# Kernel optimization log

Hardware: AMD Instinct MI355X
Metric: run time of the kernel (lower is better)

The kernel has to match this reference:

```python
import jax, jax.numpy as jnp
import numpy as np

B, N, C = 8, 1024, 1024
H = 16
D = C // H  # head_dim = 64


def apply_rope(t, cos, sin):
    # t: (B,H,N,D), cos/sin: (N, D//2). Interleaved-pair RoPE
    # (matches repeat_interleave(2) + stack(-y2,y1) in the torch code).
    tr = t.reshape(*t.shape[:-1], D // 2, 2)
    t1, t2 = tr[..., 0], tr[..., 1]
    o1 = t1 * cos - t2 * sin
    o2 = t2 * cos + t1 * sin
    return jnp.stack((o1, o2), axis=-1).reshape(t.shape)


def setup_inputs() -> dict:
    key = jax.random.key(0)
    k1, k2, k3, k4 = jax.random.split(key, 4)
    s = 0.02
    x = jax.random.normal(k1, (B, N, C), dtype=jnp.float32)
    w_qkv = jax.random.normal(k2, (C, 3 * C), dtype=jnp.float32) * s  # qkv_bias=False
    w_proj = jax.random.normal(k3, (C, C), dtype=jnp.float32) * s
    b_proj = jax.random.normal(k4, (C,), dtype=jnp.float32) * s
    return {"x": x, "w_qkv": w_qkv, "w_proj": w_proj, "b_proj": b_proj}


def reference(x, w_qkv, w_proj, b_proj):
    # QKV projection: (B,N,3C) -> (3,B,H,N,D)
    qkv = (x @ w_qkv).reshape(B, N, 3, H, D).transpose(2, 0, 3, 1, 4)
    q, k, v = qkv[0], qkv[1], qkv[2]

    # RoPE tables: pos = arange(N) (mask=None, no cls/registers)
    pos = jnp.arange(N, dtype=jnp.float32)
    omega = 1.0 / (10000.0 ** (jnp.arange(D // 2, dtype=jnp.float32) / (D / 2.0)))
    freq = pos[:, None] * omega  # (N, D//2)
    cos, sin = jnp.cos(freq), jnp.sin(freq)

    q = apply_rope(q, cos, sin)
    k = apply_rope(k, cos, sin)

    # Scaled dot-product attention (non-causal, no dropout in eval)
    scale = 1.0 / jnp.sqrt(jnp.float32(D))
    scores = jnp.einsum('bhqd,bhkd->bhqk', q, k) * scale
    attn = jax.nn.softmax(scores, axis=-1)
    out = jnp.einsum('bhqk,bhkd->bhqd', attn, v)

    # Merge heads + output projection
    out = out.transpose(0, 2, 1, 3).reshape(B, N, C)
    return out @ w_proj + b_proj
```

## Files before the change

### kernel.cpp

```cpp
#include <hip/hip_runtime.h>
#include <hip/hip_bf16.h>
#include <math.h>

#define Bsz  8
#define Nseq 1024
#define Cdim 1024
#define Hh   16
#define Dd   64

typedef short short8 __attribute__((ext_vector_type(8)));
typedef float floatx4 __attribute__((ext_vector_type(4)));

__device__ __forceinline__ unsigned short f2bf(float f) {
    __hip_bfloat16 h = __float2bfloat16(f);
    return __builtin_bit_cast(unsigned short, h);
}
__device__ __forceinline__ float b2f(unsigned short u) {
    return __uint_as_float(((unsigned)u) << 16);
}

__device__ __forceinline__ void async16(const void* g, void* l) {
    __builtin_amdgcn_global_load_lds(
        (const __attribute__((address_space(1))) unsigned int*)g,
        (__attribute__((address_space(3))) unsigned int*)l, 16, 0, 0);
}

__device__ __forceinline__ unsigned pack_bf16(float lo, float hi) {
    unsigned ulo = __float_as_uint(lo) + 0x8000u;
    unsigned uhi = __float_as_uint(hi) + 0x8000u;
    return __builtin_amdgcn_perm(uhi, ulo, 0x07060302);
}

__global__ __launch_bounds__(256) void rope_table(float2* __restrict__ tbl)
{
    int i = blockIdx.x * 256 + threadIdx.x;
    int n = i >> 5, p = i & 31;
    float omega = __expf(-(float)p * 0.2878231366242557f);
    float sv, cv;
    sincosf((float)n * omega, &sv, &cv);
    tbl[i] = make_float2(cv, sv);
}

__global__ __launch_bounds__(256) void convert_bf16(
    const float* __restrict__ in, unsigned short* __restrict__ out)
{
    int i = blockIdx.x * 256 + threadIdx.x;
    float4 v = ((const float4*)in)[i];
    ushort4 u;
    u.x = f2bf(v.x); u.y = f2bf(v.y); u.z = f2bf(v.z); u.w = f2bf(v.w);
    ((ushort4*)out)[i] = u;
}

__global__ __launch_bounds__(256) void transpose_bf16(
    const float* __restrict__ in, unsigned short* __restrict__ out, int R, int Ccols)
{
    __shared__ float T[64][65];
    int c0 = blockIdx.x * 64, r0 = blockIdx.y * 64;
    for (int i = threadIdx.x; i < 4096; i += 256) {
        int r = i >> 6, c = i & 63;
        T[r][c] = in[(size_t)(r0 + r) * Ccols + c0 + c];
    }
    __syncthreads();
    for (int i = threadIdx.x; i < 4096; i += 256) {
        int rr = i >> 6, cc = i & 63;
        out[(size_t)(c0 + rr) * R + r0 + cc] = f2bf(T[cc][rr]);
    }
}

__global__ __launch_bounds__(256) void rope_scatter(
    const unsigned short* __restrict__ qkv, const float2* __restrict__ rope,
    unsigned short* __restrict__ qb, unsigned short* __restrict__ kb)
{
    int i = blockIdx.x * 256 + threadIdx.x;
    int row = i >> 9;
    int col = (i & 511) * 4;
    int sec = col >> 10;
    int cc  = col & 1023;
    int h = cc >> 6, d = cc & 63;
    int b = row >> 10, n = row & 1023;

    ushort4 v = *(const ushort4*)(qkv + (size_t)row * 3072 + sec * 1024 + cc);
    float2 cs0 = rope[n * 32 + (d >> 1)];
    float2 cs1 = rope[n * 32 + (d >> 1) + 1];
    float x0 = b2f(v.x), x1 = b2f(v.y), x2 = b2f(v.z), x3 = b2f(v.w);
    float scale = (sec == 0) ? 0.125f : 1.f;
    ushort4 o;
    o.x = f2bf((x0 * cs0.x - x1 * cs0.y) * scale);
    o.y = f2bf((x1 * cs0.x + x0 * cs0.y) * scale);
    o.z = f2bf((x2 * cs1.x - x3 * cs1.y) * scale);
    o.w = f2bf((x3 * cs1.x + x2 * cs1.y) * scale);
    unsigned short* dst = (sec == 0) ? qb : kb;
    *(ushort4*)(dst + (((size_t)(b * Hh + h) * Nseq + n) * Dd + d)) = o;
}

__global__ __launch_bounds__(256) void transpose_vq(
    const unsigned short* __restrict__ qkv, unsigned short* __restrict__ out)
{
    __shared__ unsigned short T[64][68];
    const int nt = blockIdx.x, bh = blockIdx.y;
    const int b = bh >> 4, h = bh & 15;
    const int tid = threadIdx.x;

    for (int i = tid; i < 1024; i += 256) {
        int r = i >> 4, c4 = i & 15;
        const unsigned short* src =
            qkv + (size_t)(b * 1024 + nt * 64 + r) * 3072 + 2048 + h * 64;
        ushort4 v = ((const ushort4*)src)[c4];
        T[c4 * 4 + 0][r] = v.x;
        T[c4 * 4 + 1][r] = v.y;
        T[c4 * 4 + 2][r] = v.z;
        T[c4 * 4 + 3][r] = v.w;
    }
    __syncthreads();
    const size_t obase = (size_t)bh * Dd * Nseq + (size_t)nt * 64;
    for (int i = tid; i < 1024; i += 256) {
        int d = i >> 4, seg = i & 15;
        ushort4 v = *(const ushort4*)&T[d][seg * 4];
        *(ushort4*)(out + obase + (size_t)d * Nseq + seg * 4) = v;
    }
}

template <int MODE>
__global__ __launch_bounds__(256) void gemm_bf16(
    const unsigned short* __restrict__ A, const unsigned short* __restrict__ Bt,
    const float* __restrict__ bias,
    unsigned short* __restrict__ qkv, float* __restrict__ out)
{
    const int K = 1024;
    const int NW = (MODE == 0) ? 3072 : 1024;
    __shared__ short As[128][32];
    __shared__ short Bs[128][32];
    const int tid  = threadIdx.x;
    const int wave = tid >> 6, lane = tid & 63;
    const int ml = lane & 15, quad = lane >> 4;
    const int wm = wave >> 1, wn = wave & 1;
    const int bm = blockIdx.y * 128, bn = blockIdx.x * 128;

    const int gchunk = ((lane & 3) ^ ((lane >> 3) & 3)) * 8;
    const int srow   = lane >> 2;
    const int rslot  = (quad ^ ((ml >> 1) & 3)) * 8;

    floatx4 acc[4][4] = {};

    for (int k0 = 0; k0 < K; k0 += 32) {
        #pragma unroll
        for (int t = 0; t < 2; ++t) {
            int r0  = wave * 16 + t * 64;
            int row = r0 + srow;
            int kp  = k0 + gchunk;
            async16(A  + (size_t)(bm + row) * K + kp, &As[r0][0]);
            async16(Bt + (size_t)(bn + row) * K + kp, &Bs[r0][0]);
        }
        __syncthreads();

        short8 araw[4], braw[4];
        #pragma unroll
        for (int mi = 0; mi < 4; ++mi)
            araw[mi] = *(const short8*)&As[wm * 64 + mi * 16 + ml][rslot];
        #pragma unroll
        for (int ni = 0; ni < 4; ++ni)
            braw[ni] = *(const short8*)&Bs[wn * 64 + ni * 16 + ml][rslot];
        #pragma unroll
        for (int mi = 0; mi < 4; ++mi)
            #pragma unroll
            for (int ni = 0; ni < 4; ++ni)
                acc[mi][ni] = __builtin_amdgcn_mfma_f32_16x16x32_bf16(
                    araw[mi], braw[ni], acc[mi][ni], 0, 0, 0);
        __syncthreads();
    }

    if (MODE == 0) {
        #pragma unroll
        for (int ni = 0; ni < 4; ++ni) {
            int col = bn + wn * 64 + ni * 16 + ml;
            #pragma unroll
            for (int mi = 0; mi < 4; ++mi)
                #pragma unroll
                for (int r = 0; r < 4; ++r) {
                    int row = bm + wm * 64 + mi * 16 + quad * 4 + r;
                    qkv[(size_t)row * NW + col] = f2bf(acc[mi][ni][r]);
                }
        }
    } else {
        #pragma unroll
        for (int ni = 0; ni < 4; ++ni) {
            int col = bn + wn * 64 + ni * 16 + ml;
            float bv = bias[col];
            #pragma unroll
            for (int mi = 0; mi < 4; ++mi)
                #pragma unroll
                for (int r = 0; r < 4; ++r) {
                    int row = bm + wm * 64 + mi * 16 + quad * 4 + r;
                    out[(size_t)row * NW + col] = acc[mi][ni][r] + bv;
                }
        }
    }
}

__global__ __launch_bounds__(256) void attn_flash_mfma(
    const unsigned short* __restrict__ qb, const unsigned short* __restrict__ kb,
    const unsigned short* __restrict__ vt, unsigned short* __restrict__ ao)
{
    const int bh  = blockIdx.x;
    const int qt  = blockIdx.y;
    const int tid = threadIdx.x;
    const int wave = tid >> 6, lane = tid & 63;
    const int ml = lane & 15, quad = lane >> 4;
    const int lr = lane >> 3;
    const int lc = ((lane & 7) ^ lr) * 8;

    __shared__ short Qs[128][64];
    __shared__ short Ks[64][64];
    __shared__ short Vs[64][64];
    __shared__ short Ps[4][32][72];

    const size_t hbase = (size_t)bh * (Nseq * Dd);
    const int q0 = qt * 128;
    const int wq = wave * 32;
    const int wk = wave * 16;

    #pragma unroll
    for (int t = 0; t < 4; ++t)
        async16(qb + hbase + (size_t)(q0 + wq + t * 8 + lr) * 64 + lc, &Qs[wq + t * 8][0]);

    float l0 = 0.f, l1 = 0.f;
    floatx4 o[2][4] = {};

    for (int kt = 0; kt < 16; ++kt) {
        __syncthreads();
        const int k0r = kt * 64;
        async16(kb + hbase + (size_t)(k0r + wk + lr) * 64 + lc,     &Ks[wk][0]);
        async16(kb + hbase + (size_t)(k0r + wk + 8 + lr) * 64 + lc, &Ks[wk + 8][0]);
        async16(vt + ((size_t)bh * 64 + wk + lr) * Nseq + k0r + lc,     &Vs[wk][0]);
        async16(vt + ((size_t)bh * 64 + wk + 8 + lr) * Nseq + k0r + lc, &Vs[wk + 8][0]);
        __syncthreads();

        floatx4 st[2][4] = {};
        #pragma unroll
        for (int ks = 0; ks < 2; ++ks) {
            const int sl = ((ks * 4 + quad) ^ (ml & 7)) * 8;
            short8 qf0 = *(const short8*)&Qs[wq + ml][sl];
            short8 qf1 = *(const short8*)&Qs[wq + 16 + ml][sl];
            #pragma unroll
            for (int kbk = 0; kbk < 4; ++kbk) {
                short8 kf = *(const short8*)&Ks[kbk * 16 + ml][sl];
                st[0][kbk] = __builtin_amdgcn_mfma_f32_16x16x32_bf16(kf, qf0, st[0][kbk], 0, 0, 0);
                st[1][kbk] = __builtin_amdgcn_mfma_f32_16x16x32_bf16(kf, qf1, st[1][kbk], 0, 0, 0);
            }
        }

        #pragma unroll
        for (int qg = 0; qg < 2; ++qg) {
            float lacc = 0.f;
            #pragma unroll
            for (int kbk = 0; kbk < 4; ++kbk) {
                float e0 = __expf(st[qg][kbk][0]);
                float e1 = __expf(st[qg][kbk][1]);
                float e2 = __expf(st[qg][kbk][2]);
                float e3 = __expf(st[qg][kbk][3]);
                lacc += (e0 + e1) + (e2 + e3);
                uint2 pk;
                pk.x = pack_bf16(e0, e1);
                pk.y = pack_bf16(e2, e3);
                *(uint2*)&Ps[wave][qg * 16 + ml][kbk * 16 + quad * 4] = pk;
            }
            if (qg == 0) l0 += lacc; else l1 += lacc;
        }

        #pragma unroll
        for (int ks = 0; ks < 2; ++ks) {
            const int sl = ((ks * 4 + quad) ^ (ml & 7)) * 8;
            short8 pf0 = *(const short8*)&Ps[wave][ml][ks * 32 + quad * 8];
            short8 pf1 = *(const short8*)&Ps[wave][16 + ml][ks * 32 + quad * 8];
            #pragma unroll
            for (int nt = 0; nt < 4; ++nt) {
                short8 vf = *(const short8*)&Vs[nt * 16 + ml][sl];
                o[0][nt] = __builtin_amdgcn_mfma_f32_16x16x32_bf16(pf0, vf, o[0][nt], 0, 0, 0);
                o[1][nt] = __builtin_amdgcn_mfma_f32_16x16x32_bf16(pf1, vf, o[1][nt], 0, 0, 0);
            }
        }
    }

    l0 += __shfl_xor(l0, 16);
    l0 += __shfl_xor(l0, 32);
    l1 += __shfl_xor(l1, 16);
    l1 += __shfl_xor(l1, 32);

    const int b = bh >> 4, h = bh & 15;
    #pragma unroll
    for (int qg = 0; qg < 2; ++qg) {
        float lsrc = (qg == 0) ? l0 : l1;
        #pragma unroll
        for (int r = 0; r < 4; ++r) {
            float lq = __shfl(lsrc, quad * 4 + r);
            float inv = 1.f / lq;
            int q = q0 + wq + qg * 16 + quad * 4 + r;
            size_t rowbase = ((size_t)(b * Nseq + q)) * Cdim + h * Dd;
            #pragma unroll
            for (int nt = 0; nt < 4; ++nt)
                ao[rowbase + nt * 16 + ml] = f2bf(o[qg][nt][r] * inv);
        }
    }
}

extern "C" void kernel_launch(void* const* d_in, const int* in_sizes, int n_in,
                              void* d_out, int out_size, void* d_ws, size_t ws_size,
                              hipStream_t stream) {
    const float* x      = (const float*)d_in[0];
    const float* w_qkv  = (const float*)d_in[1];
    const float* w_proj = (const float*)d_in[2];
    const float* b_proj = (const float*)d_in[3];
    float* out = (float*)d_out;

    const size_t M8 = (size_t)8 * 1024 * 1024;
    unsigned short* qb     = (unsigned short*)d_ws;
    unsigned short* kb     = qb + M8;
    unsigned short* vt     = kb + M8;
    unsigned short* xb     = vt + M8;
    unsigned short* wqkvt  = xb + M8;
    unsigned short* wprojt = wqkvt + 3 * 1024 * 1024;
    float2*         rope   = (float2*)(wprojt + 1024 * 1024);
    unsigned short* qkvws  = (unsigned short*)(rope + 32768);
    unsigned short* aob    = xb;

    rope_table<<<128, 256, 0, stream>>>(rope);
    convert_bf16<<<8192, 256, 0, stream>>>(x, xb);
    transpose_bf16<<<dim3(48, 16), 256, 0, stream>>>(w_qkv, wqkvt, 1024, 3072);
    transpose_bf16<<<dim3(16, 16), 256, 0, stream>>>(w_proj, wprojt, 1024, 1024);

    gemm_bf16<0><<<dim3(24, 64), 256, 0, stream>>>(xb, wqkvt, nullptr, qkvws, nullptr);

    rope_scatter<<<16384, 256, 0, stream>>>(qkvws, rope, qb, kb);
    transpose_vq<<<dim3(16, 128), 256, 0, stream>>>(qkvws, vt);

    attn_flash_mfma<<<dim3(128, 8), 256, 0, stream>>>(qb, kb, vt, aob);

    gemm_bf16<1><<<dim3(8, 64), 256, 0, stream>>>(aob, wprojt, b_proj, nullptr, out);
}
```

Baseline: 275.1 us.

## Merge prep and scatter kernels, hoist Q fragments, overlap K/V loads in attention

```diff
diff --git a/kernel.cpp b/kernel.cpp
--- a/kernel.cpp
+++ b/kernel.cpp
@@ -31,92 +31,111 @@
     return __builtin_amdgcn_perm(uhi, ulo, 0x07060302);
 }
 
-__global__ __launch_bounds__(256) void rope_table(float2* __restrict__ tbl)
-{
-    int i = blockIdx.x * 256 + threadIdx.x;
-    int n = i >> 5, p = i & 31;
-    float omega = __expf(-(float)p * 0.2878231366242557f);
-    float sv, cv;
-    sincosf((float)n * omega, &sv, &cv);
-    tbl[i] = make_float2(cv, sv);
-}
-
-__global__ __launch_bounds__(256) void convert_bf16(
-    const float* __restrict__ in, unsigned short* __restrict__ out)
-{
-    int i = blockIdx.x * 256 + threadIdx.x;
-    float4 v = ((const float4*)in)[i];
-    ushort4 u;
-    u.x = f2bf(v.x); u.y = f2bf(v.y); u.z = f2bf(v.z); u.w = f2bf(v.w);
-    ((ushort4*)out)[i] = u;
-}
-
-__global__ __launch_bounds__(256) void transpose_bf16(
-    const float* __restrict__ in, unsigned short* __restrict__ out, int R, int Ccols)
+__global__ __launch_bounds__(256) void prep(
+    const float* __restrict__ x, const float* __restrict__ w_qkv,
+    const float* __restrict__ w_proj,
+    unsigned short* __restrict__ xb, unsigned short* __restrict__ wqkvt,
+    unsigned short* __restrict__ wprojt, float2* __restrict__ rope)
 {
     __shared__ float T[64][65];
-    int c0 = blockIdx.x * 64, r0 = blockIdx.y * 64;
-    for (int i = threadIdx.x; i < 4096; i += 256) {
-        int r = i >> 6, c = i & 63;
-        T[r][c] = in[(size_t)(r0 + r) * Ccols + c0 + c];
-    }
-    __syncthreads();
-    for (int i = threadIdx.x; i < 4096; i += 256) {
-        int rr = i >> 6, cc = i & 63;
-        out[(size_t)(c0 + rr) * R + r0 + cc] = f2bf(T[cc][rr]);
-    }
-}
-
-__global__ __launch_bounds__(256) void rope_scatter(
+    const int blk = blockIdx.x;
+    const int tid = threadIdx.x;
+
+    if (blk < 8192) {
+        int i = blk * 256 + tid;
+        float4 v = ((const float4*)x)[i];
+        ushort4 u;
+        u.x = f2bf(v.x); u.y = f2bf(v.y); u.z = f2bf(v.z); u.w = f2bf(v.w);
+        ((ushort4*)xb)[i] = u;
+        return;
+    }
+    if (blk < 9216) {
+        const float* in;
+        unsigned short* out;
+        int R = 1024, Ccols, c0, r0;
+        if (blk < 8960) {
+            int b2 = blk - 8192;
+            in = w_qkv; out = wqkvt; Ccols = 3072;
+            c0 = (b2 % 48) * 64; r0 = (b2 / 48) * 64;
+        } else {
+            int b2 = blk - 8960;
+            in = w_proj; out = wprojt; Ccols = 1024;
+            c0 = (b2 % 16) * 64; r0 = (b2 / 16) * 64;
+        }
+        for (int i = tid; i < 4096; i += 256) {
+            int r = i >> 6, c = i & 63;
+            T[r][c] = in[(size_t)(r0 + r) * Ccols + c0 + c];
+        }
+        __syncthreads();
+        for (int i = tid; i < 4096; i += 256) {
+            int rr = i >> 6, cc = i & 63;
+            out[(size_t)(c0 + rr) * R + r0 + cc] = f2bf(T[cc][rr]);
+        }
+        return;
+    }
+    {
+        int i = (blk - 9216) * 256 + tid;
+        int n = i >> 5, p = i & 31;
+        float omega = __expf(-(float)p * 0.2878231366242557f);
+        float sv, cv;
+        sincosf((float)n * omega, &sv, &cv);
+        rope[i] = make_float2(cv, sv);
+    }
+}
+
+__global__ __launch_bounds__(256) void scatter(
     const unsigned short* __restrict__ qkv, const float2* __restrict__ rope,
-    unsigned short* __restrict__ qb, unsigned short* __restrict__ kb)
-{
-    int i = blockIdx.x * 256 + threadIdx.x;
-    int row = i >> 9;
-    int col = (i & 511) * 4;
-    int sec = col >> 10;
-    int cc  = col & 1023;
-    int h = cc >> 6, d = cc & 63;
-    int b = row >> 10, n = row & 1023;
-
-    ushort4 v = *(const ushort4*)(qkv + (size_t)row * 3072 + sec * 1024 + cc);
-    float2 cs0 = rope[n * 32 + (d >> 1)];
-    float2 cs1 = rope[n * 32 + (d >> 1) + 1];
-    float x0 = b2f(v.x), x1 = b2f(v.y), x2 = b2f(v.z), x3 = b2f(v.w);
-    float scale = (sec == 0) ? 0.125f : 1.f;
-    ushort4 o;
-    o.x = f2bf((x0 * cs0.x - x1 * cs0.y) * scale);
-    o.y = f2bf((x1 * cs0.x + x0 * cs0.y) * scale);
-    o.z = f2bf((x2 * cs1.x - x3 * cs1.y) * scale);
-    o.w = f2bf((x3 * cs1.x + x2 * cs1.y) * scale);
-    unsigned short* dst = (sec == 0) ? qb : kb;
-    *(ushort4*)(dst + (((size_t)(b * Hh + h) * Nseq + n) * Dd + d)) = o;
-}
-
-__global__ __launch_bounds__(256) void transpose_vq(
-    const unsigned short* __restrict__ qkv, unsigned short* __restrict__ out)
+    unsigned short* __restrict__ qb, unsigned short* __restrict__ kb,
+    unsigned short* __restrict__ vt)
 {
     __shared__ unsigned short T[64][68];
-    const int nt = blockIdx.x, bh = blockIdx.y;
-    const int b = bh >> 4, h = bh & 15;
+    const int blk = blockIdx.x;
     const int tid = threadIdx.x;
 
-    for (int i = tid; i < 1024; i += 256) {
-        int r = i >> 4, c4 = i & 15;
-        const unsigned short* src =
-            qkv + (size_t)(b * 1024 + nt * 64 + r) * 3072 + 2048 + h * 64;
-        ushort4 v = ((const ushort4*)src)[c4];
-        T[c4 * 4 + 0][r] = v.x;
-        T[c4 * 4 + 1][r] = v.y;
-        T[c4 * 4 + 2][r] = v.z;
-        T[c4 * 4 + 3][r] = v.w;
-    }
-    __syncthreads();
-    const size_t obase = (size_t)bh * Dd * Nseq + (size_t)nt * 64;
-    for (int i = tid; i < 1024; i += 256) {
-        int d = i >> 4, seg = i & 15;
-        ushort4 v = *(const ushort4*)&T[d][seg * 4];
-        *(ushort4*)(out + obase + (size_t)d * Nseq + seg * 4) = v;
+    if (blk < 16384) {
+        int i = blk * 256 + tid;
+        int row = i >> 9;
+        int col = (i & 511) * 4;
+        int sec = col >> 10;
+        int cc  = col & 1023;
+        int h = cc >> 6, d = cc & 63;
+        int b = row >> 10, n = row & 1023;
+
+        ushort4 v = *(const ushort4*)(qkv + (size_t)row * 3072 + sec * 1024 + cc);
+        float2 cs0 = rope[n * 32 + (d >> 1)];
+        float2 cs1 = rope[n * 32 + (d >> 1) + 1];
+        float x0 = b2f(v.x), x1 = b2f(v.y), x2 = b2f(v.z), x3 = b2f(v.w);
+        float scale = (sec == 0) ? 0.125f : 1.f;
+        ushort4 o;
+        o.x = f2bf((x0 * cs0.x - x1 * cs0.y) * scale);
+        o.y = f2bf((x1 * cs0.x + x0 * cs0.y) * scale);
+        o.z = f2bf((x2 * cs1.x - x3 * cs1.y) * scale);
+        o.w = f2bf((x3 * cs1.x + x2 * cs1.y) * scale);
+        unsigned short* dst = (sec == 0) ? qb : kb;
+        *(ushort4*)(dst + (((size_t)(b * Hh + h) * Nseq + n) * Dd + d)) = o;
+        return;
+    }
+    {
+        int b2 = blk - 16384;
+        int nt = b2 & 15, bh = b2 >> 4;
+        int b = bh >> 4, h = bh & 15;
+        for (int i = tid; i < 1024; i += 256) {
+            int r = i >> 4, c4 = i & 15;
+            const unsigned short* src =
+                qkv + (size_t)(b * 1024 + nt * 64 + r) * 3072 + 2048 + h * 64;
+            ushort4 v = ((const ushort4*)src)[c4];
+            T[c4 * 4 + 0][r] = v.x;
+            T[c4 * 4 + 1][r] = v.y;
+            T[c4 * 4 + 2][r] = v.z;
+            T[c4 * 4 + 3][r] = v.w;
+        }
+        __syncthreads();
+        const size_t obase = (size_t)bh * Dd * Nseq + (size_t)nt * 64;
+        for (int i = tid; i < 1024; i += 256) {
+            int d = i >> 4, seg = i & 15;
+            ushort4 v = *(const ushort4*)&T[d][seg * 4];
+            *(ushort4*)(vt + obase + (size_t)d * Nseq + seg * 4) = v;
+        }
     }
 }
 
@@ -215,6 +234,7 @@
     __shared__ short Ps[4][32][72];
 
     const size_t hbase = (size_t)bh * (Nseq * Dd);
+    const size_t vbase = (size_t)bh * 64;
     const int q0 = qt * 128;
     const int wq = wave * 32;
     const int wk = wave * 16;
@@ -222,30 +242,35 @@
     #pragma unroll
     for (int t = 0; t < 4; ++t)
         async16(qb + hbase + (size_t)(q0 + wq + t * 8 + lr) * 64 + lc, &Qs[wq + t * 8][0]);
+    async16(kb + hbase + (size_t)(wk + lr) * 64 + lc,     &Ks[wk][0]);
+    async16(kb + hbase + (size_t)(wk + 8 + lr) * 64 + lc, &Ks[wk + 8][0]);
+    __syncthreads();
+
+    short8 qfr[2][2];
+    #pragma unroll
+    for (int ks = 0; ks < 2; ++ks) {
+        const int sl = ((ks * 4 + quad) ^ (ml & 7)) * 8;
+        qfr[ks][0] = *(const short8*)&Qs[wq + ml][sl];
+        qfr[ks][1] = *(const short8*)&Qs[wq + 16 + ml][sl];
+    }
 
     float l0 = 0.f, l1 = 0.f;
     floatx4 o[2][4] = {};
 
     for (int kt = 0; kt < 16; ++kt) {
-        __syncthreads();
         const int k0r = kt * 64;
-        async16(kb + hbase + (size_t)(k0r + wk + lr) * 64 + lc,     &Ks[wk][0]);
-        async16(kb + hbase + (size_t)(k0r + wk + 8 + lr) * 64 + lc, &Ks[wk + 8][0]);
-        async16(vt + ((size_t)bh * 64 + wk + lr) * Nseq + k0r + lc,     &Vs[wk][0]);
-        async16(vt + ((size_t)bh * 64 + wk + 8 + lr) * Nseq + k0r + lc, &Vs[wk + 8][0]);
-        __syncthreads();
+        async16(vt + (vbase + wk + lr) * Nseq + k0r + lc,     &Vs[wk][0]);
+        async16(vt + (vbase + wk + 8 + lr) * Nseq + k0r + lc, &Vs[wk + 8][0]);
 
         floatx4 st[2][4] = {};
         #pragma unroll
         for (int ks = 0; ks < 2; ++ks) {
             const int sl = ((ks * 4 + quad) ^ (ml & 7)) * 8;
-            short8 qf0 = *(const short8*)&Qs[wq + ml][sl];
-            short8 qf1 = *(const short8*)&Qs[wq + 16 + ml][sl];
             #pragma unroll
             for (int kbk = 0; kbk < 4; ++kbk) {
                 short8 kf = *(const short8*)&Ks[kbk * 16 + ml][sl];
-                st[0][kbk] = __builtin_amdgcn_mfma_f32_16x16x32_bf16(kf, qf0, st[0][kbk], 0, 0, 0);
-                st[1][kbk] = __builtin_amdgcn_mfma_f32_16x16x32_bf16(kf, qf1, st[1][kbk], 0, 0, 0);
+                st[0][kbk] = __builtin_amdgcn_mfma_f32_16x16x32_bf16(kf, qfr[ks][0], st[0][kbk], 0, 0, 0);
+                st[1][kbk] = __builtin_amdgcn_mfma_f32_16x16x32_bf16(kf, qfr[ks][1], st[1][kbk], 0, 0, 0);
             }
         }
 
@@ -266,6 +291,13 @@
             }
             if (qg == 0) l0 += lacc; else l1 += lacc;
         }
+        __syncthreads();
+
+        if (kt < 15) {
+            const int k1r = k0r + 64;
+            async16(kb + hbase + (size_t)(k1r + wk + lr) * 64 + lc,     &Ks[wk][0]);
+            async16(kb + hbase + (size_t)(k1r + wk + 8 + lr) * 64 + lc, &Ks[wk + 8][0]);
+        }
 
         #pragma unroll
         for (int ks = 0; ks < 2; ++ks) {
@@ -279,6 +311,8 @@
                 o[1][nt] = __builtin_amdgcn_mfma_f32_16x16x32_bf16(pf1, vf, o[1][nt], 0, 0, 0);
             }
         }
+        if (kt < 15)
+            __syncthreads();
     }
 
     l0 += __shfl_xor(l0, 16);
@@ -323,15 +357,11 @@
     unsigned short* qkvws  = (unsigned short*)(rope + 32768);
     unsigned short* aob    = xb;
 
-    rope_table<<<128, 256, 0, stream>>>(rope);
-    convert_bf16<<<8192, 256, 0, stream>>>(x, xb);
-    transpose_bf16<<<dim3(48, 16), 256, 0, stream>>>(w_qkv, wqkvt, 1024, 3072);
-    transpose_bf16<<<dim3(16, 16), 256, 0, stream>>>(w_proj, wprojt, 1024, 1024);
+    prep<<<9344, 256, 0, stream>>>(x, w_qkv, w_proj, xb, wqkvt, wprojt, rope);
 
     gemm_bf16<0><<<dim3(24, 64), 256, 0, stream>>>(xb, wqkvt, nullptr, qkvws, nullptr);
 
-    rope_scatter<<<16384, 256, 0, stream>>>(qkvws, rope, qb, kb);
-    transpose_vq<<<dim3(16, 128), 256, 0, stream>>>(qkvws, vt);
+    scatter<<<18432, 256, 0, stream>>>(qkvws, rope, qb, kb, vt);
 
     attn_flash_mfma<<<dim3(128, 8), 256, 0, stream>>>(qb, kb, vt, aob);
 
```

Measured after the change: 255.2 us. 1.08x faster.
